# Kernel tuning notes

Hardware: AMD Instinct MI355X
Metric: run time of the kernel (lower is better)

Reference implementation:

```python
import jax, jax.numpy as jnp
import numpy as np

B, S, D, A = 8, 4096, 128, 128


def _pos_encoding(seq_len, dim):
    # sin/cos positional encoding, same construction as the torch buffer
    pos = np.arange(seq_len, dtype=np.float32)[:, None]
    div = np.exp(np.arange(0, dim, 2, dtype=np.float32) * (-np.log(10000.0) / dim))
    pe = np.zeros((seq_len, dim), dtype=np.float32)
    pe[:, 0::2] = np.sin(pos * div)
    pe[:, 1::2] = np.cos(pos * div)
    return jnp.asarray(pe)


def setup_inputs() -> dict:
    key = jax.random.key(0)
    ks = jax.random.split(key, 7)
    sc = 1.0 / np.sqrt(D)
    return {
        "x": jax.random.normal(ks[0], (B, S, D), dtype=jnp.float32),
        "Wq": jax.random.normal(ks[1], (D, A), dtype=jnp.float32) * sc,
        "bq": jnp.zeros((A,), dtype=jnp.float32),
        "Wk": jax.random.normal(ks[2], (D, A), dtype=jnp.float32) * sc,
        "bk": jnp.zeros((A,), dtype=jnp.float32),
        "Wv": jax.random.normal(ks[3], (D, A), dtype=jnp.float32) * sc,
        "bv": jnp.zeros((A,), dtype=jnp.float32),
    }


def reference(x, Wq, bq, Wk, bk, Wv, bv):
    b, s, d = x.shape
    pe = _pos_encoding(s, d)  # [S, D]
    xp = x + pe[None]  # broadcast add of positional encoding
    q = xp @ Wq + bq  # [B, S, A]
    k = xp @ Wk + bk
    v = xp @ Wv + bv
    scale = 1.0 / jnp.sqrt(jnp.asarray(Wq.shape[1], dtype=jnp.float32))
    scores = jnp.einsum("bsa,bta->bst", q, k) * scale  # [B, S, S]
    weights = jax.nn.softmax(scores, axis=-1)
    out = jnp.einsum("bst,bta->bsa", weights, v)  # [B, S, A]
    return out
```

## Files before the change

### kernel.cpp

```cpp
#include <hip/hip_runtime.h>

#define BB 8
#define SS 4096
#define DD 128

typedef __attribute__((ext_vector_type(8))) short v8s;
typedef __attribute__((ext_vector_type(4))) short v4s;
typedef __attribute__((ext_vector_type(4))) float v4f;

__device__ __forceinline__ unsigned short f2bf(float f) {
    unsigned int u = __float_as_uint(f);
    u += 0x7fffu + ((u >> 16) & 1u);
    return (unsigned short)(u >> 16);
}
__device__ __forceinline__ float bf2f(unsigned short s) {
    return __uint_as_float(((unsigned int)s) << 16);
}
__device__ __forceinline__ unsigned int pk_bf16(float a, float b) {
    unsigned int ua = __float_as_uint(a) + 0x8000u;
    unsigned int ub = __float_as_uint(b) + 0x8000u;
    return __builtin_amdgcn_perm(ub, ua, 0x07060302u);
}

#if !defined(__HIP_DEVICE_COMPILE__)
#define MFMA_BF16_32(a, b, c) (c)
#else
#define MFMA_BF16_32(a, b, c) __builtin_amdgcn_mfma_f32_16x16x32_bf16((a), (b), (c), 0, 0, 0)
#endif

#define EXP2F(x) exp2f(x)
#define QSCALE 0.12751743f
#define FIXM 24.0f

__global__ __launch_bounds__(256) void prep_w_kernel(
    const float* __restrict__ Wq, const float* __restrict__ Wk,
    const float* __restrict__ Wv, unsigned short* __restrict__ Wt)
{
    int id = blockIdx.x * 256 + threadIdx.x;
    int w = id >> 14;
    int n = (id >> 7) & 127;
    int k = id & 127;
    const float* W = (w == 0) ? Wq : (w == 1) ? Wk : Wv;
    Wt[id] = f2bf(W[k * 128 + n]);
}

__global__ __launch_bounds__(256, 3) void proj_kernel(
    const float* __restrict__ x, const unsigned short* __restrict__ Wt,
    const float* __restrict__ bq, const float* __restrict__ bk,
    const float* __restrict__ bv,
    unsigned short* __restrict__ qo, unsigned short* __restrict__ ko,
    unsigned short* __restrict__ vo)
{
    __shared__ __attribute__((aligned(16))) unsigned short w_lds[128 * 136];
    __shared__ __attribute__((aligned(16))) unsigned short o_lds[9216];

    const int tid = threadIdx.x;
    const int wave = tid >> 6;
    const int lane = tid & 63;
    const int quad = lane >> 4;
    const int l15 = lane & 15;
    const int bid = blockIdx.x;
    const int mat = bid % 3;
    const int rbase = (bid / 3) * 64;

    const unsigned short* Wp = Wt + (mat << 14);
#pragma unroll
    for (int it = 0; it < 8; ++it) {
        int id = it * 256 + tid;
        int n = id >> 4, c8 = id & 15;
        *(v8s*)(w_lds + n * 136 + c8 * 8) = *(const v8s*)(Wp + n * 128 + c8 * 8);
    }

    const int flatrow = rbase + wave * 16 + l15;
    const int srow = flatrow & 4095;
    v8s af[4];
#pragma unroll
    for (int kc = 0; kc < 4; ++kc) {
        const int kbase = kc * 32 + quad * 8;
        const v4f* xp = (const v4f*)(x + (size_t)flatrow * DD + kbase);
        v4f x0 = xp[0], x1 = xp[1];
        float xv[8] = {x0[0], x0[1], x0[2], x0[3], x1[0], x1[1], x1[2], x1[3]};
        v8s a;
#pragma unroll
        for (int j = 0; j < 8; ++j) {
            int d = kbase + j;
            float freq = __expf((float)(d & ~1) * -0.07195578415606394f);
            float arg = (float)srow * freq;
            float pe = (d & 1) ? __cosf(arg) : __sinf(arg);
            a[j] = (short)f2bf(xv[j] + pe);
        }
        af[kc] = a;
    }

    const float* bias = (mat == 0) ? bq : (mat == 1) ? bk : bv;
    __syncthreads();

#pragma unroll
    for (int nb = 0; nb < 8; ++nb) {
        const int col = nb * 16 + l15;
        v4f acc = {0.f, 0.f, 0.f, 0.f};
#pragma unroll
        for (int kc = 0; kc < 4; ++kc) {
            v8s bf = *(const v8s*)(w_lds + col * 136 + kc * 32 + quad * 8);
            acc = MFMA_BF16_32(af[kc], bf, acc);
        }
        float bval = bias[col];
#pragma unroll
        for (int reg = 0; reg < 4; ++reg) {
            int lr = wave * 16 + quad * 4 + reg;
            float val = acc[reg] + bval;
            if (mat == 0) {
                o_lds[lr * 136 + col] = f2bf(val * QSCALE);
            } else if (mat == 1) {
                o_lds[lr * 136 + col] = f2bf(val);
            } else {
                o_lds[col * 72 + lr] = f2bf(val);
            }
        }
    }
    __syncthreads();

    if (mat <= 1) {
        unsigned short* out = (mat == 0) ? qo : ko;
#pragma unroll
        for (int it = 0; it < 4; ++it) {
            int id = it * 256 + tid;
            int r = id >> 4, c8 = id & 15;
            *(v8s*)(out + (size_t)(rbase + r) * DD + c8 * 8) =
                *(const v8s*)(o_lds + r * 136 + c8 * 8);
        }
    } else {
        const int b0 = rbase >> 12, s0 = rbase & 4095;
#pragma unroll
        for (int it = 0; it < 4; ++it) {
            int id = it * 256 + tid;
            int a = id >> 3, c = id & 7;
            *(v8s*)(vo + ((size_t)(b0 * 128 + a)) * SS + s0 + c * 8) =
                *(const v8s*)(o_lds + a * 72 + c * 8);
        }
    }
}

#define HKEYS 2048
__global__ __launch_bounds__(256, 2) void flash_kernel(
    const unsigned short* __restrict__ qg,
    const unsigned short* __restrict__ kg,
    const unsigned short* __restrict__ vg,
    float* __restrict__ out,
    unsigned short* __restrict__ o2,
    float* __restrict__ statl)
{
    __shared__ __attribute__((aligned(16))) unsigned short k_lds[64 * 128];
    __shared__ __attribute__((aligned(16))) unsigned short v_lds[128 * 64];

    const int tid = threadIdx.x;
    const int wave = tid >> 6;
    const int lane = tid & 63;
    const int quad = lane >> 4;
    const int l15 = lane & 15;
    const int bid = blockIdx.x;
    const int b = bid & 7;
    const int half = (bid >> 3) & 1;
    const int qt = bid >> 4;
    const int qbase = qt * 128 + wave * 32;

    v8s qfA[4], qfB[4];
    {
        const size_t rA = (size_t)(b * SS + qbase + l15) * DD;
        const size_t rB = (size_t)(b * SS + qbase + 16 + l15) * DD;
#pragma unroll
        for (int kc = 0; kc < 4; ++kc) {
            qfA[kc] = *(const v8s*)(qg + rA + kc * 32 + quad * 8);
            qfB[kc] = *(const v8s*)(qg + rB + kc * 32 + quad * 8);
        }
    }

    v4f oA[8], oB[8];
#pragma unroll
    for (int i = 0; i < 8; ++i) {
        oA[i] = (v4f){0.f, 0.f, 0.f, 0.f};
        oB[i] = (v4f){0.f, 0.f, 0.f, 0.f};
    }
    float lA = 0.f, lB = 0.f;

    const unsigned short* kb = kg + (size_t)b * SS * DD + (size_t)half * HKEYS * DD;
    const unsigned short* vb = vg + (size_t)b * DD * SS + half * HKEYS;

    v8s kr[4], vr[4];
    const int kr_r = tid >> 4, kr_c = tid & 15;
    const int vr_a = tid >> 3, vr_c = tid & 7;
#pragma unroll
    for (int it = 0; it < 4; ++it) {
        kr[it] = *(const v8s*)(kb + (size_t)(kr_r + it * 16) * DD + kr_c * 8);
        vr[it] = *(const v8s*)(vb + (size_t)(vr_a + it * 32) * SS + vr_c * 8);
    }

    for (int kt = 0; kt < HKEYS / 64; ++kt) {
        __syncthreads();
#pragma unroll
        for (int it = 0; it < 4; ++it) {
            int r = kr_r + it * 16;
            *(v8s*)(k_lds + r * 128 + (((kr_c) ^ (r & 7)) << 3)) = kr[it];
            int a = vr_a + it * 32;
            int c4 = vr_c * 2;
            v4s lo = {vr[it][0], vr[it][1], vr[it][2], vr[it][3]};
            v4s hi = {vr[it][4], vr[it][5], vr[it][6], vr[it][7]};
            *(v4s*)(v_lds + a * 64 + (((c4)     ^ (a & 15)) << 2)) = lo;
            *(v4s*)(v_lds + a * 64 + (((c4 + 1) ^ (a & 15)) << 2)) = hi;
        }
        __syncthreads();

        if (kt + 1 < HKEYS / 64) {
            const unsigned short* kn = kb + (size_t)(kt + 1) * 64 * DD;
            const unsigned short* vn = vb + (kt + 1) * 64;
#pragma unroll
            for (int it = 0; it < 4; ++it) {
                kr[it] = *(const v8s*)(kn + (size_t)(kr_r + it * 16) * DD + kr_c * 8);
                vr[it] = *(const v8s*)(vn + (size_t)(vr_a + it * 32) * SS + vr_c * 8);
            }
        }

        v4f sA[4], sB[4];
#pragma unroll
        for (int c = 0; c < 4; ++c) {
            v4f aA = {0.f, 0.f, 0.f, 0.f};
            v4f aB = {0.f, 0.f, 0.f, 0.f};
#pragma unroll
            for (int kc = 0; kc < 4; ++kc) {
                v8s af = *(const v8s*)(k_lds + (c * 16 + l15) * 128 +
                                       (((kc * 4 + quad) ^ (l15 & 7)) << 3));
                aA = MFMA_BF16_32(af, qfA[kc], aA);
                aB = MFMA_BF16_32(af, qfB[kc], aB);
            }
            sA[c] = aA;
            sB[c] = aB;
        }

        union { v8s v[2]; unsigned int u[8]; } PA, PB;
#pragma unroll
        for (int c = 0; c < 4; ++c) {
            float a0 = EXP2F(sA[c][0] - FIXM), a1 = EXP2F(sA[c][1] - FIXM);
            float a2 = EXP2F(sA[c][2] - FIXM), a3 = EXP2F(sA[c][3] - FIXM);
            lA += (a0 + a1) + (a2 + a3);
            PA.u[c * 2]     = pk_bf16(a0, a1);
            PA.u[c * 2 + 1] = pk_bf16(a2, a3);
            float b0 = EXP2F(sB[c][0] - FIXM), b1 = EXP2F(sB[c][1] - FIXM);
            float b2 = EXP2F(sB[c][2] - FIXM), b3 = EXP2F(sB[c][3] - FIXM);
            lB += (b0 + b1) + (b2 + b3);
            PB.u[c * 2]     = pk_bf16(b0, b1);
            PB.u[c * 2 + 1] = pk_bf16(b2, b3);
        }

#pragma unroll
        for (int kc2 = 0; kc2 < 2; ++kc2) {
#pragma unroll
            for (int ab = 0; ab < 8; ++ab) {
                const unsigned short* vrow = v_lds + (ab * 16 + l15) * 64;
                union { v8s v; v4s h[2]; } bf;
                bf.h[0] = *(const v4s*)(vrow + (((kc2 * 8 + quad)     ^ l15) << 2));
                bf.h[1] = *(const v4s*)(vrow + (((kc2 * 8 + 4 + quad) ^ l15) << 2));
                oA[ab] = MFMA_BF16_32(PA.v[kc2], bf.v, oA[ab]);
                oB[ab] = MFMA_BF16_32(PB.v[kc2], bf.v, oB[ab]);
            }
        }
    }

    lA += __shfl_xor(lA, 16, 64);
    lA += __shfl_xor(lA, 32, 64);
    lB += __shfl_xor(lB, 16, 64);
    lB += __shfl_xor(lB, 32, 64);
    if (quad == 0) {
        int qi = half * (BB * SS) + b * SS + qbase + l15;
        statl[qi] = lA;
        statl[qi + 16] = lB;
    }
#pragma unroll
    for (int ab = 0; ab < 8; ++ab)
#pragma unroll
        for (int reg = 0; reg < 4; ++reg) {
            int srA = qbase + quad * 4 + reg;
            size_t iA = (size_t)(b * SS + srA) * DD + ab * 16 + l15;
            size_t iB = (size_t)(b * SS + srA + 16) * DD + ab * 16 + l15;
            if (half == 0) {
                out[iA] = oA[ab][reg];
                out[iB] = oB[ab][reg];
            } else {
                o2[iA] = f2bf(oA[ab][reg]);
                o2[iB] = f2bf(oB[ab][reg]);
            }
        }
}

__global__ __launch_bounds__(256) void combine_kernel(
    float* __restrict__ out, const unsigned short* __restrict__ o2,
    const float* __restrict__ statl)
{
    int id = blockIdx.x * 256 + threadIdx.x;
    int row = id >> 5;
    int c = (id & 31) * 4;
    float l1 = statl[row], l2 = statl[BB * SS + row];
    float inv = 1.0f / (l1 + l2);
    size_t base = (size_t)row * DD + c;
    v4f o1 = *(v4f*)(out + base);
    v4s p2 = *(const v4s*)(o2 + base);
    v4f r;
#pragma unroll
    for (int j = 0; j < 4; ++j)
        r[j] = (o1[j] + bf2f((unsigned short)p2[j])) * inv;
    *(v4f*)(out + base) = r;
}

extern "C" void kernel_launch(void* const* d_in, const int* in_sizes, int n_in,
                              void* d_out, int out_size, void* d_ws, size_t ws_size,
                              hipStream_t stream)
{
    const float* x  = (const float*)d_in[0];
    const float* Wq = (const float*)d_in[1];
    const float* bq = (const float*)d_in[2];
    const float* Wk = (const float*)d_in[3];
    const float* bk = (const float*)d_in[4];
    const float* Wv = (const float*)d_in[5];
    const float* bv = (const float*)d_in[6];
    float* out = (float*)d_out;

    unsigned short* Wt = (unsigned short*)d_ws;
    unsigned short* q  = Wt + 49152;
    unsigned short* k  = q + (size_t)BB * SS * DD;
    unsigned short* vT = k + (size_t)BB * SS * DD;
    unsigned short* O2 = vT + (size_t)BB * SS * DD;
    float* statl = (float*)(O2 + (size_t)BB * SS * DD);

    hipLaunchKernelGGL(prep_w_kernel, dim3(192), dim3(256), 0, stream, Wq, Wk, Wv, Wt);
    hipLaunchKernelGGL(proj_kernel, dim3(BB * SS / 64 * 3), dim3(256), 0, stream,
                       x, Wt, bq, bk, bv, q, k, vT);
    hipLaunchKernelGGL(flash_kernel, dim3(SS / 128 * 2 * BB), dim3(256), 0, stream,
                       q, k, vT, out, O2, statl);
    hipLaunchKernelGGL(combine_kernel, dim3(BB * SS * DD / 4 / 256), dim3(256), 0, stream,
                       out, O2, statl);
}
```

Before: 193.7 us.

## Double-buffer flash K/V LDS tiles, compute row sums via MFMA, drop proj LDS staging

The flash kernel now keeps two LDS buffers for K and V. Storing the next tile overlaps compute on the current one, so each key tile needs one barrier instead of two. The softmax denominator is now accumulated with an MFMA against a vector of bf16 ones, replacing the scalar adds and the cross-lane shuffles. Other changes: precomputed swizzle offsets, the amdgcn exp2 builtin, and the projection kernel reading weights straight from global memory with no LDS staging or barrier. Doubling the LDS may lower occupancy. The bf16-rounded row sums change the numerics slightly.

```diff
diff --git a/kernel.cpp b/kernel.cpp
--- a/kernel.cpp
+++ b/kernel.cpp
@@ -28,7 +28,14 @@
 #define MFMA_BF16_32(a, b, c) __builtin_amdgcn_mfma_f32_16x16x32_bf16((a), (b), (c), 0, 0, 0)
 #endif
 
+#if !defined(__HIP_DEVICE_COMPILE__)
 #define EXP2F(x) exp2f(x)
+#elif __has_builtin(__builtin_amdgcn_exp2f)
+#define EXP2F(x) __builtin_amdgcn_exp2f(x)
+#else
+#define EXP2F(x) exp2f(x)
+#endif
+
 #define QSCALE 0.12751743f
 #define FIXM 24.0f
 
@@ -44,14 +51,13 @@
     Wt[id] = f2bf(W[k * 128 + n]);
 }
 
-__global__ __launch_bounds__(256, 3) void proj_kernel(
+__global__ __launch_bounds__(256) void proj_kernel(
     const float* __restrict__ x, const unsigned short* __restrict__ Wt,
     const float* __restrict__ bq, const float* __restrict__ bk,
     const float* __restrict__ bv,
     unsigned short* __restrict__ qo, unsigned short* __restrict__ ko,
     unsigned short* __restrict__ vo)
 {
-    __shared__ __attribute__((aligned(16))) unsigned short w_lds[128 * 136];
     __shared__ __attribute__((aligned(16))) unsigned short o_lds[9216];
 
     const int tid = threadIdx.x;
@@ -63,14 +69,6 @@
     const int mat = bid % 3;
     const int rbase = (bid / 3) * 64;
 
-    const unsigned short* Wp = Wt + (mat << 14);
-#pragma unroll
-    for (int it = 0; it < 8; ++it) {
-        int id = it * 256 + tid;
-        int n = id >> 4, c8 = id & 15;
-        *(v8s*)(w_lds + n * 136 + c8 * 8) = *(const v8s*)(Wp + n * 128 + c8 * 8);
-    }
-
     const int flatrow = rbase + wave * 16 + l15;
     const int srow = flatrow & 4095;
     v8s af[4];
@@ -92,8 +90,8 @@
         af[kc] = a;
     }
 
+    const unsigned short* Wp = Wt + (mat << 14);
     const float* bias = (mat == 0) ? bq : (mat == 1) ? bk : bv;
-    __syncthreads();
 
 #pragma unroll
     for (int nb = 0; nb < 8; ++nb) {
@@ -101,7 +99,7 @@
         v4f acc = {0.f, 0.f, 0.f, 0.f};
 #pragma unroll
         for (int kc = 0; kc < 4; ++kc) {
-            v8s bf = *(const v8s*)(w_lds + col * 136 + kc * 32 + quad * 8);
+            v8s bf = *(const v8s*)(Wp + col * 128 + kc * 32 + quad * 8);
             acc = MFMA_BF16_32(af[kc], bf, acc);
         }
         float bval = bias[col];
@@ -121,12 +119,12 @@
     __syncthreads();
 
     if (mat <= 1) {
-        unsigned short* out = (mat == 0) ? qo : ko;
+        unsigned short* outp = (mat == 0) ? qo : ko;
 #pragma unroll
         for (int it = 0; it < 4; ++it) {
             int id = it * 256 + tid;
             int r = id >> 4, c8 = id & 15;
-            *(v8s*)(out + (size_t)(rbase + r) * DD + c8 * 8) =
+            *(v8s*)(outp + (size_t)(rbase + r) * DD + c8 * 8) =
                 *(const v8s*)(o_lds + r * 136 + c8 * 8);
         }
     } else {
@@ -142,6 +140,7 @@
 }
 
 #define HKEYS 2048
+#define NT (HKEYS / 64)
 __global__ __launch_bounds__(256, 2) void flash_kernel(
     const unsigned short* __restrict__ qg,
     const unsigned short* __restrict__ kg,
@@ -150,8 +149,8 @@
     unsigned short* __restrict__ o2,
     float* __restrict__ statl)
 {
-    __shared__ __attribute__((aligned(16))) unsigned short k_lds[64 * 128];
-    __shared__ __attribute__((aligned(16))) unsigned short v_lds[128 * 64];
+    __shared__ __attribute__((aligned(16))) unsigned short k_lds[2][8192];
+    __shared__ __attribute__((aligned(16))) unsigned short v_lds[2][8192];
 
     const int tid = threadIdx.x;
     const int wave = tid >> 6;
@@ -181,45 +180,51 @@
         oA[i] = (v4f){0.f, 0.f, 0.f, 0.f};
         oB[i] = (v4f){0.f, 0.f, 0.f, 0.f};
     }
-    float lA = 0.f, lB = 0.f;
+    v4f laccA = {0.f, 0.f, 0.f, 0.f}, laccB = {0.f, 0.f, 0.f, 0.f};
+
+    v8s ones;
+#pragma unroll
+    for (int j = 0; j < 8; ++j) ones[j] = (short)0x3F80;
 
     const unsigned short* kb = kg + (size_t)b * SS * DD + (size_t)half * HKEYS * DD;
     const unsigned short* vb = vg + (size_t)b * DD * SS + half * HKEYS;
 
+    int kbo[4], vbo[2][2];
+#pragma unroll
+    for (int kc = 0; kc < 4; ++kc)
+        kbo[kc] = l15 * 128 + (((kc * 4 + quad) ^ (l15 & 7)) << 3);
+#pragma unroll
+    for (int kc2 = 0; kc2 < 2; ++kc2) {
+        vbo[kc2][0] = l15 * 64 + (((kc2 * 8 + quad) ^ l15) << 2);
+        vbo[kc2][1] = l15 * 64 + (((kc2 * 8 + 4 + quad) ^ l15) << 2);
+    }
+    const int kr_r = tid >> 4, kr_c = tid & 15;
+    const int va0 = tid >> 3, vc4 = (tid & 7) * 2;
+    const int kwb = kr_r * 128 + ((kr_c ^ (kr_r & 7)) << 3);
+    const int vwb0 = va0 * 64 + ((vc4 ^ (va0 & 15)) << 2);
+    const int vwb1 = va0 * 64 + (((vc4 + 1) ^ (va0 & 15)) << 2);
+
     v8s kr[4], vr[4];
-    const int kr_r = tid >> 4, kr_c = tid & 15;
-    const int vr_a = tid >> 3, vr_c = tid & 7;
-#pragma unroll
-    for (int it = 0; it < 4; ++it) {
-        kr[it] = *(const v8s*)(kb + (size_t)(kr_r + it * 16) * DD + kr_c * 8);
-        vr[it] = *(const v8s*)(vb + (size_t)(vr_a + it * 32) * SS + vr_c * 8);
-    }
-
-    for (int kt = 0; kt < HKEYS / 64; ++kt) {
-        __syncthreads();
+    auto load_tile = [&](int t) {
+        const unsigned short* kp = kb + (size_t)t * 64 * DD;
+        const unsigned short* vp = vb + t * 64;
 #pragma unroll
         for (int it = 0; it < 4; ++it) {
-            int r = kr_r + it * 16;
-            *(v8s*)(k_lds + r * 128 + (((kr_c) ^ (r & 7)) << 3)) = kr[it];
-            int a = vr_a + it * 32;
-            int c4 = vr_c * 2;
+            kr[it] = *(const v8s*)(kp + (size_t)(kr_r + it * 16) * DD + kr_c * 8);
+            vr[it] = *(const v8s*)(vp + (size_t)(va0 + it * 32) * SS + (tid & 7) * 8);
+        }
+    };
+    auto store_tile = [&](int p) {
+#pragma unroll
+        for (int it = 0; it < 4; ++it) {
+            *(v8s*)(&k_lds[p][kwb + it * 2048]) = kr[it];
             v4s lo = {vr[it][0], vr[it][1], vr[it][2], vr[it][3]};
             v4s hi = {vr[it][4], vr[it][5], vr[it][6], vr[it][7]};
-            *(v4s*)(v_lds + a * 64 + (((c4)     ^ (a & 15)) << 2)) = lo;
-            *(v4s*)(v_lds + a * 64 + (((c4 + 1) ^ (a & 15)) << 2)) = hi;
-        }
-        __syncthreads();
-
-        if (kt + 1 < HKEYS / 64) {
-            const unsigned short* kn = kb + (size_t)(kt + 1) * 64 * DD;
-            const unsigned short* vn = vb + (kt + 1) * 64;
-#pragma unroll
-            for (int it = 0; it < 4; ++it) {
-                kr[it] = *(const v8s*)(kn + (size_t)(kr_r + it * 16) * DD + kr_c * 8);
-                vr[it] = *(const v8s*)(vn + (size_t)(vr_a + it * 32) * SS + vr_c * 8);
-            }
-        }
-
+            *(v4s*)(&v_lds[p][vwb0 + it * 2048]) = lo;
+            *(v4s*)(&v_lds[p][vwb1 + it * 2048]) = hi;
+        }
+    };
+    auto compute = [&](int p) {
         v4f sA[4], sB[4];
 #pragma unroll
         for (int c = 0; c < 4; ++c) {
@@ -227,52 +232,65 @@
             v4f aB = {0.f, 0.f, 0.f, 0.f};
 #pragma unroll
             for (int kc = 0; kc < 4; ++kc) {
-                v8s af = *(const v8s*)(k_lds + (c * 16 + l15) * 128 +
-                                       (((kc * 4 + quad) ^ (l15 & 7)) << 3));
+                v8s af = *(const v8s*)(&k_lds[p][c * 2048 + kbo[kc]]);
                 aA = MFMA_BF16_32(af, qfA[kc], aA);
                 aB = MFMA_BF16_32(af, qfB[kc], aB);
             }
             sA[c] = aA;
             sB[c] = aB;
         }
-
         union { v8s v[2]; unsigned int u[8]; } PA, PB;
 #pragma unroll
         for (int c = 0; c < 4; ++c) {
             float a0 = EXP2F(sA[c][0] - FIXM), a1 = EXP2F(sA[c][1] - FIXM);
             float a2 = EXP2F(sA[c][2] - FIXM), a3 = EXP2F(sA[c][3] - FIXM);
-            lA += (a0 + a1) + (a2 + a3);
             PA.u[c * 2]     = pk_bf16(a0, a1);
             PA.u[c * 2 + 1] = pk_bf16(a2, a3);
             float b0 = EXP2F(sB[c][0] - FIXM), b1 = EXP2F(sB[c][1] - FIXM);
             float b2 = EXP2F(sB[c][2] - FIXM), b3 = EXP2F(sB[c][3] - FIXM);
-            lB += (b0 + b1) + (b2 + b3);
             PB.u[c * 2]     = pk_bf16(b0, b1);
             PB.u[c * 2 + 1] = pk_bf16(b2, b3);
         }
-
 #pragma unroll
         for (int kc2 = 0; kc2 < 2; ++kc2) {
+            laccA = MFMA_BF16_32(PA.v[kc2], ones, laccA);
+            laccB = MFMA_BF16_32(PB.v[kc2], ones, laccB);
 #pragma unroll
             for (int ab = 0; ab < 8; ++ab) {
-                const unsigned short* vrow = v_lds + (ab * 16 + l15) * 64;
                 union { v8s v; v4s h[2]; } bf;
-                bf.h[0] = *(const v4s*)(vrow + (((kc2 * 8 + quad)     ^ l15) << 2));
-                bf.h[1] = *(const v4s*)(vrow + (((kc2 * 8 + 4 + quad) ^ l15) << 2));
+                bf.h[0] = *(const v4s*)(&v_lds[p][ab * 1024 + vbo[kc2][0]]);
+                bf.h[1] = *(const v4s*)(&v_lds[p][ab * 1024 + vbo[kc2][1]]);
                 oA[ab] = MFMA_BF16_32(PA.v[kc2], bf.v, oA[ab]);
                 oB[ab] = MFMA_BF16_32(PB.v[kc2], bf.v, oB[ab]);
             }
         }
-    }
-
-    lA += __shfl_xor(lA, 16, 64);
-    lA += __shfl_xor(lA, 32, 64);
-    lB += __shfl_xor(lB, 16, 64);
-    lB += __shfl_xor(lB, 32, 64);
-    if (quad == 0) {
-        int qi = half * (BB * SS) + b * SS + qbase + l15;
-        statl[qi] = lA;
-        statl[qi + 16] = lB;
+    };
+
+    load_tile(0);
+    store_tile(0);
+    load_tile(1);
+    __syncthreads();
+#pragma unroll 1
+    for (int kt = 0; kt < NT; kt += 2) {
+        store_tile(1);
+        if (kt + 2 < NT) load_tile(kt + 2);
+        compute(0);
+        __syncthreads();
+        if (kt + 2 < NT) {
+            store_tile(0);
+            if (kt + 3 < NT) load_tile(kt + 3);
+        }
+        compute(1);
+        __syncthreads();
+    }
+
+    if (l15 == 0) {
+        int qi = half * (BB * SS) + b * SS + qbase;
+#pragma unroll
+        for (int reg = 0; reg < 4; ++reg) {
+            statl[qi + quad * 4 + reg] = laccA[reg];
+            statl[qi + 16 + quad * 4 + reg] = laccB[reg];
+        }
     }
 #pragma unroll
     for (int ab = 0; ab < 8; ++ab)
```

Result: faster. 187.1 us (-3.4%).
